# Optimization experiments

Hardware: AMD Instinct MI355X
Metric: run time of the kernel (lower is better)

The kernel has to match this reference:

```python
import jax, jax.numpy as jnp
import numpy as np

DIM = 192
HID = 128
EPS = 1e-8
ITERS = 3
LN_EPS = 1e-5
SCALE = DIM ** (-0.5)


def layer_norm(x, w, b):
    mu = x.mean(axis=-1, keepdims=True)
    var = ((x - mu) ** 2).mean(axis=-1, keepdims=True)
    return (x - mu) * jax.lax.rsqrt(var + LN_EPS) * w + b


def gru_cell(x, h, Wih, Whh, bih, bhh):
    # PyTorch GRUCell: gates ordered (r, z, n)
    gx = x @ Wih.T + bih          # [M, 3*DIM]
    gh = h @ Whh.T + bhh          # [M, 3*DIM]
    xr, xz, xn = jnp.split(gx, 3, axis=-1)
    hr, hz, hn = jnp.split(gh, 3, axis=-1)
    r = jax.nn.sigmoid(xr + hr)
    z = jax.nn.sigmoid(xz + hz)
    n = jnp.tanh(xn + r * hn)
    return (1.0 - z) * n + z * h


def setup_inputs() -> dict:
    key = jax.random.key(0)
    ks = jax.random.split(key, 12)
    B, N, K = 64, 4096, 11
    s = 0.02
    return {
        "inputs": jax.random.normal(ks[0], (B, N, DIM), jnp.float32),
        "noise": jax.random.normal(ks[1], (B, K, DIM), jnp.float32),
        "slots_mu": jax.random.normal(ks[2], (1, 1, DIM), jnp.float32),
        "slots_sigma": jax.random.uniform(ks[3], (1, 1, DIM), jnp.float32),
        "ln_in_w": jnp.ones((DIM,), jnp.float32),
        "ln_in_b": jnp.zeros((DIM,), jnp.float32),
        "ln_slots_w": jnp.ones((DIM,), jnp.float32),
        "ln_slots_b": jnp.zeros((DIM,), jnp.float32),
        "ln_mlp_w": jnp.ones((DIM,), jnp.float32),
        "ln_mlp_b": jnp.zeros((DIM,), jnp.float32),
        "Wq": jax.random.normal(ks[4], (DIM, DIM), jnp.float32) * s,
        "bq": jnp.zeros((DIM,), jnp.float32),
        "Wk": jax.random.normal(ks[5], (DIM, DIM), jnp.float32) * s,
        "bk": jnp.zeros((DIM,), jnp.float32),
        "Wv": jax.random.normal(ks[6], (DIM, DIM), jnp.float32) * s,
        "bv": jnp.zeros((DIM,), jnp.float32),
        "gru_Wih": jax.random.normal(ks[7], (3 * DIM, DIM), jnp.float32) * s,
        "gru_Whh": jax.random.normal(ks[8], (3 * DIM, DIM), jnp.float32) * s,
        "gru_bih": jnp.zeros((3 * DIM,), jnp.float32),
        "gru_bhh": jnp.zeros((3 * DIM,), jnp.float32),
        "mlp_W1": jax.random.normal(ks[9], (DIM, HID), jnp.float32) * s,
        "mlp_b1": jnp.zeros((HID,), jnp.float32),
        "mlp_W2": jax.random.normal(ks[10], (HID, DIM), jnp.float32) * s,
        "mlp_b2": jnp.zeros((DIM,), jnp.float32),
        "n_slots": 11,
    }


def reference(inputs, noise, slots_mu, slots_sigma,
              ln_in_w, ln_in_b, ln_slots_w, ln_slots_b, ln_mlp_w, ln_mlp_b,
              Wq, bq, Wk, bk, Wv, bv,
              gru_Wih, gru_Whh, gru_bih, gru_bhh,
              mlp_W1, mlp_b1, mlp_W2, mlp_b2, n_slots):
    B, N, _ = inputs.shape
    # slots ~ Normal(mu, sigma), reparameterized with fixed noise
    slots = slots_mu + slots_sigma * noise            # [B, K, D]
    x = layer_norm(inputs, ln_in_w, ln_in_b)
    key_vec = x @ Wk + bk                             # [B, N, D]
    val_vec = x @ Wv + bv                             # [B, N, D]
    attn_output = None
    for _ in range(ITERS):
        slots_prev = slots
        s_n = layer_norm(slots, ln_slots_w, ln_slots_b)
        q = s_n @ Wq + bq                             # [B, K, D]
        dots = jnp.einsum('bkd,bnd->bkn', q, key_vec) * SCALE
        attn = jax.nn.softmax(dots, axis=1) + EPS     # softmax over slots axis
        attn_output = attn
        attn = attn / attn.sum(axis=-1, keepdims=True)
        updates = jnp.einsum('bnd,bkn->bkd', val_vec, attn)
        h = gru_cell(updates.reshape(-1, DIM), slots_prev.reshape(-1, DIM),
                     gru_Wih, gru_Whh, gru_bih, gru_bhh)
        slots = h.reshape(B, -1, DIM)
        m = layer_norm(slots, ln_mlp_w, ln_mlp_b)
        m = jax.nn.relu(m @ mlp_W1 + mlp_b1) @ mlp_W2 + mlp_b2
        slots = slots + m
    return (slots, attn_output)
```

## Files before the change

kernel.cpp:

```cpp
#include <hip/hip_runtime.h>
#include <hip/hip_bf16.h>
#include <cstdint>
#include <cstddef>

#define DIM 192
#define NSL 11
#define NB 64
#define NN 4096
#define HIDN 128
#define NCHP 16
#define TROWS 32
#define NT 8
#define LN_EPS 1e-5f
#define EPS_A 1e-8f
#define SCALE_Q 0.07216878364870323f

__device__ __forceinline__ float wred(float v) {
#pragma unroll
  for (int m = 32; m; m >>= 1) v += __shfl_xor(v, m, 64);
  return v;
}

typedef const __attribute__((address_space(1))) void gas_void;
typedef __attribute__((address_space(3))) void las_void;
__device__ __forceinline__ void gload_lds16(const void* g, void* l) {
  __builtin_amdgcn_global_load_lds((gas_void*)g, (las_void*)l, 16, 0, 0);
}

__global__ __launch_bounds__(256) void k_tr(
    const float* __restrict__ Wih, const float* __restrict__ Whh, const float* __restrict__ Wk,
    float* __restrict__ WihT, float* __restrict__ WhhT, float* __restrict__ WkT) {
  __shared__ float t[64][65];
  int tile = blockIdx.x;
  const float* src; float* dst; int R, C;
  if (tile < 27)      { src = Wih; dst = WihT; R = 576; C = 192; }
  else if (tile < 54) { src = Whh; dst = WhhT; R = 576; C = 192; tile -= 27; }
  else                { src = Wk;  dst = WkT;  R = 192; C = 192; tile -= 54; }
  const int ntc = C >> 6;
  const int tr = tile / ntc, tc = tile % ntc;
  const int lane = threadIdx.x & 63, w = threadIdx.x >> 6;
#pragma unroll
  for (int i = 0; i < 16; ++i) {
    int row = w * 16 + i;
    t[row][lane] = src[(size_t)(tr * 64 + row) * C + tc * 64 + lane];
  }
  __syncthreads();
#pragma unroll
  for (int i = 0; i < 16; ++i) {
    int row = w * 16 + i;
    dst[(size_t)(tc * 64 + row) * R + tr * 64 + lane] = t[lane][row];
  }
}

__global__ __launch_bounds__(192) void k_prep(
    const float* __restrict__ lnw, const float* __restrict__ lnb,
    const float* __restrict__ Wq, const float* __restrict__ bq,
    const float* __restrict__ WkT, const float* __restrict__ bk,
    const float* __restrict__ xw, const float* __restrict__ xb,
    const float* __restrict__ noise, const float* __restrict__ mu0, const float* __restrict__ sig,
    float* __restrict__ slots_ws,
    float* __restrict__ qt, float* __restrict__ t0g, float* __restrict__ cpg) {
  const int b = blockIdx.x, kg = blockIdx.y, tid = threadIdx.x;
  const int k0 = kg * 3, kcnt = (kg == 3) ? 2 : 3;
  const int wave = tid >> 6, lane = tid & 63;
  const int j = tid;
  __shared__ __align__(16) float sn[3][DIM];
  __shared__ __align__(16) float qb[3][DIM];
  __shared__ float red[3][3][2];

#pragma unroll
  for (int kk = 0; kk < 3; ++kk) {
    if (kk < kcnt) {
      float v = mu0[j] + sig[j] * noise[(size_t)(b * NSL + k0 + kk) * DIM + j];
      sn[kk][j] = v;
      slots_ws[(size_t)(b * NSL + k0 + kk) * DIM + j] = v;
    } else sn[kk][j] = 0.f;
  }
  __syncthreads();

  for (int kk = wave; kk < 3; kk += 3) {
    float a = sn[kk][lane], c = sn[kk][lane + 64], e = sn[kk][lane + 128];
    float s = wred(a + c + e), ss = wred(a * a + c * c + e * e);
    float mu = s * (1.0f / DIM), var = ss * (1.0f / DIM) - mu * mu;
    float rstd = rsqrtf(var + LN_EPS);
    sn[kk][lane]       = (a - mu) * rstd * lnw[lane]       + lnb[lane];
    sn[kk][lane + 64]  = (c - mu) * rstd * lnw[lane + 64]  + lnb[lane + 64];
    sn[kk][lane + 128] = (e - mu) * rstd * lnw[lane + 128] + lnb[lane + 128];
  }
  __syncthreads();

  float acc[3];
  const float bj = bq[j];
#pragma unroll
  for (int kk = 0; kk < 3; ++kk) acc[kk] = bj;
  for (int d = 0; d < DIM; d += 4) {
    float w0 = Wq[(d + 0) * DIM + j], w1 = Wq[(d + 1) * DIM + j];
    float w2 = Wq[(d + 2) * DIM + j], w3 = Wq[(d + 3) * DIM + j];
#pragma unroll
    for (int kk = 0; kk < 3; ++kk) {
      float4 s4 = *(const float4*)&sn[kk][d];
      acc[kk] = fmaf(s4.w, w3, fmaf(s4.z, w2, fmaf(s4.y, w1, fmaf(s4.x, w0, acc[kk]))));
    }
  }
#pragma unroll
  for (int kk = 0; kk < 3; ++kk) qb[kk][j] = acc[kk];
  __syncthreads();

  float qk[3];
#pragma unroll
  for (int kk = 0; kk < 3; ++kk) qk[kk] = 0.f;
  for (int d = 0; d < DIM; d += 4) {
    float w0 = WkT[(d + 0) * DIM + j], w1 = WkT[(d + 1) * DIM + j];
    float w2 = WkT[(d + 2) * DIM + j], w3 = WkT[(d + 3) * DIM + j];
#pragma unroll
    for (int kk = 0; kk < 3; ++kk) {
      float4 q4 = *(const float4*)&qb[kk][d];
      qk[kk] = fmaf(q4.w, w3, fmaf(q4.z, w2, fmaf(q4.y, w1, fmaf(q4.x, w0, qk[kk]))));
    }
  }
  const float wj = xw[j], bxj = xb[j], bkj = bk[j];
#pragma unroll
  for (int kk = 0; kk < 3; ++kk) {
    float qtv = SCALE_Q * wj * qk[kk];
    if (kk < kcnt) qt[(size_t)(b * NSL + k0 + kk) * DIM + j] = qtv;
    float r1 = wred(qtv);
    float r2 = wred(SCALE_Q * (bxj * qk[kk] + qb[kk][j] * bkj));
    if (lane == 0) { red[wave][kk][0] = r1; red[wave][kk][1] = r2; }
  }
  __syncthreads();
  if (tid < kcnt) {
    t0g[b * NSL + k0 + tid] = red[0][tid][0] + red[1][tid][0] + red[2][tid][0];
    cpg[b * NSL + k0 + tid] = red[0][tid][1] + red[1][tid][1] + red[2][tid][1];
  }
}

__global__ __launch_bounds__(256) __attribute__((amdgpu_waves_per_eu(4, 4))) void k_iter(
    const float* __restrict__ x, const float* __restrict__ qt,
    const float* __restrict__ t0g, const float* __restrict__ cpg,
    float* __restrict__ attn_out, float* __restrict__ P1p,
    float* __restrict__ S_p, float* __restrict__ m1_p) {
  __shared__ __align__(16) float xs[TROWS * DIM];
  __shared__ __align__(16) float qs[NSL * DIM];
  __shared__ __align__(16) float a_lds[TROWS][12];
  __shared__ float rs_lds[TROWS];
  __shared__ float t0s[NSL], cps[NSL];
  __shared__ float redS[4][NSL], redM[4][NSL];

  const int b = blockIdx.x, ch = blockIdx.y, tid = threadIdx.x;
  const int lane = tid & 63, wv = tid >> 6;
  const int widx = tid & 15, g = tid >> 4;

  const float* xbase = x + ((size_t)b * NN + ch * 256) * DIM;

#pragma unroll
  for (int i = 0; i < 6; ++i) {
    int c = i * 4 + wv;
    gload_lds16(xbase + c * 256 + lane * 4, &xs[c * 256]);
  }
  {
    const float4* src = (const float4*)(qt + (size_t)b * NSL * DIM);
    float4* dst = (float4*)qs;
    dst[tid] = src[tid];
    dst[256 + tid] = src[256 + tid];
    if (tid < 16) dst[512 + tid] = src[512 + tid];
  }
  if (tid < NSL) { t0s[tid] = t0g[b * NSL + tid]; cps[tid] = cpg[b * NSL + tid]; }

  float acc[3][NSL], sS[NSL], sM[NSL];
#pragma unroll
  for (int k = 0; k < NSL; ++k) {
    acc[0][k] = 0.f; acc[1][k] = 0.f; acc[2][k] = 0.f;
    sS[k] = 0.f; sM[k] = 0.f;
  }

#pragma unroll 1
  for (int T = 0; T < NT; ++T) {
    if (T == 0) {
      __syncthreads();
    } else {
      __syncthreads();
      const float* src = xbase + (size_t)T * TROWS * DIM;
#pragma unroll
      for (int i = 0; i < 6; ++i) {
        int c = i * 4 + wv;
        gload_lds16(src + c * 256 + lane * 4, &xs[c * 256]);
      }
      asm volatile("s_waitcnt vmcnt(0)" ::: "memory");
      __builtin_amdgcn_s_barrier();
    }

    float dot[2][NSL], st_s[2], st_ss[2];
#pragma unroll
    for (int rr = 0; rr < 2; ++rr) {
      st_s[rr] = 0.f; st_ss[rr] = 0.f;
#pragma unroll
      for (int k = 0; k < NSL; ++k) dot[rr][k] = 0.f;
    }
#pragma unroll
    for (int w = 0; w < 3; ++w) {
      const int c4 = widx + 16 * w;
      float4 xr[2];
#pragma unroll
      for (int rr = 0; rr < 2; ++rr) {
        xr[rr] = ((const float4*)xs)[(2 * g + rr) * 48 + c4];
        st_s[rr] += (xr[rr].x + xr[rr].y) + (xr[rr].z + xr[rr].w);
        st_ss[rr] = fmaf(xr[rr].x, xr[rr].x, fmaf(xr[rr].y, xr[rr].y,
                    fmaf(xr[rr].z, xr[rr].z, fmaf(xr[rr].w, xr[rr].w, st_ss[rr]))));
      }
#pragma unroll
      for (int k = 0; k < NSL; ++k) {
        float4 qv = *(const float4*)&qs[k * DIM + 4 * c4];
#pragma unroll
        for (int rr = 0; rr < 2; ++rr)
          dot[rr][k] = fmaf(xr[rr].w, qv.w, fmaf(xr[rr].z, qv.z,
                       fmaf(xr[rr].y, qv.y, fmaf(xr[rr].x, qv.x, dot[rr][k]))));
      }
    }
#pragma unroll
    for (int m = 1; m <= 8; m <<= 1) {
#pragma unroll
      for (int rr = 0; rr < 2; ++rr) {
        st_s[rr] += __shfl_xor(st_s[rr], m, 64);
        st_ss[rr] += __shfl_xor(st_ss[rr], m, 64);
#pragma unroll
        for (int k = 0; k < NSL; ++k) dot[rr][k] += __shfl_xor(dot[rr][k], m, 64);
      }
    }
    if ((widx & 7) == 0) {
      const int hi = widx >> 3;
      const int r = 2 * g + hi;
      float dsel[NSL];
#pragma unroll
      for (int k = 0; k < NSL; ++k) dsel[k] = (widx == 0) ? dot[0][k] : dot[1][k];
      float sts  = (widx == 0) ? st_s[0]  : st_s[1];
      float stss = (widx == 0) ? st_ss[0] : st_ss[1];
      float mu = sts * (1.0f / DIM);
      float var = stss * (1.0f / DIM) - mu * mu;
      float rstd = rsqrtf(var + LN_EPS);
      float murstd = mu * rstd;
      float dv[NSL];
#pragma unroll
      for (int k = 0; k < NSL; ++k) dv[k] = fmaf(rstd, dsel[k], fmaf(-murstd, t0s[k], cps[k]));
      float mx = dv[0];
#pragma unroll
      for (int k = 1; k < NSL; ++k) mx = fmaxf(mx, dv[k]);
      float es[NSL], sum = 0.f;
#pragma unroll
      for (int k = 0; k < NSL; ++k) { es[k] = __expf(dv[k] - mx); sum += es[k]; }
      float inv = 1.0f / sum;
#pragma unroll
      for (int k = 0; k < NSL; ++k) {
        float a = fmaf(es[k], inv, EPS_A);
        a_lds[r][k] = a;
        sS[k] += a;
        sM[k] = fmaf(a, murstd, sM[k]);
      }
      rs_lds[r] = rstd;
    }
    asm volatile("s_waitcnt lgkmcnt(0)" ::: "memory");
    __builtin_amdgcn_s_barrier();

    {
      int idx = tid;
      attn_out[((size_t)(b * NSL + (idx >> 5))) * NN + ch * 256 + T * TROWS + (idx & 31)]
          = a_lds[idx & 31][idx >> 5];
      idx = tid + 256;
      if (idx < NSL * TROWS)
        attn_out[((size_t)(b * NSL + (idx >> 5))) * NN + ch * 256 + T * TROWS + (idx & 31)]
            = a_lds[idx & 31][idx >> 5];
    }
#pragma unroll 4
    for (int i = 0; i < 8; ++i) {
      const int r = 4 * i + wv;
      float rst = rs_lds[r];
      float4 a0 = *(const float4*)&a_lds[r][0];
      float4 a1 = *(const float4*)&a_lds[r][4];
      float4 a2 = *(const float4*)&a_lds[r][8];
#pragma unroll
      for (int j = 0; j < 3; ++j) {
        const int col = lane + 64 * j;
        float t1 = rst * xs[r * DIM + col];
        acc[j][0]  = fmaf(a0.x, t1, acc[j][0]);
        acc[j][1]  = fmaf(a0.y, t1, acc[j][1]);
        acc[j][2]  = fmaf(a0.z, t1, acc[j][2]);
        acc[j][3]  = fmaf(a0.w, t1, acc[j][3]);
        acc[j][4]  = fmaf(a1.x, t1, acc[j][4]);
        acc[j][5]  = fmaf(a1.y, t1, acc[j][5]);
        acc[j][6]  = fmaf(a1.z, t1, acc[j][6]);
        acc[j][7]  = fmaf(a1.w, t1, acc[j][7]);
        acc[j][8]  = fmaf(a2.x, t1, acc[j][8]);
        acc[j][9]  = fmaf(a2.y, t1, acc[j][9]);
        acc[j][10] = fmaf(a2.z, t1, acc[j][10]);
      }
    }
  }

  __syncthreads();
  float* accbuf = &xs[0];
  const int slot = tid & 127;
  if (wv < 2) {
#pragma unroll
    for (int j = 0; j < 3; ++j)
#pragma unroll
      for (int k = 0; k < NSL; ++k)
        accbuf[slot * 33 + j * 11 + k] = acc[j][k];
  }
  __syncthreads();
  if (wv >= 2) {
#pragma unroll
    for (int j = 0; j < 3; ++j)
#pragma unroll
      for (int k = 0; k < NSL; ++k)
        accbuf[slot * 33 + j * 11 + k] += acc[j][k];
  }
  __syncthreads();
  if (tid < DIM) {
    const int l = tid & 63, j = tid >> 6;
#pragma unroll
    for (int k = 0; k < NSL; ++k) {
      float v = accbuf[l * 33 + j * 11 + k] + accbuf[(64 + l) * 33 + j * 11 + k];
      P1p[(((size_t)b * NCHP + ch) * NSL + k) * DIM + tid] = v;
    }
  }
#pragma unroll
  for (int k = 0; k < NSL; ++k) { sS[k] = wred(sS[k]); sM[k] = wred(sM[k]); }
  if (lane == 0) {
#pragma unroll
    for (int k = 0; k < NSL; ++k) { redS[wv][k] = sS[k]; redM[wv][k] = sM[k]; }
  }
  __syncthreads();
  if (tid < NSL) {
    S_p[((size_t)b * NCHP + ch) * NSL + tid]  = redS[0][tid] + redS[1][tid] + redS[2][tid] + redS[3][tid];
    m1_p[((size_t)b * NCHP + ch) * NSL + tid] = redM[0][tid] + redM[1][tid] + redM[2][tid] + redM[3][tid];
  }
}

#define TPBS 768
__global__ __launch_bounds__(TPBS) void k_step(
    const float* __restrict__ P1p, const float* __restrict__ m1_p, const float* __restrict__ S_p,
    const float* __restrict__ xw, const float* __restrict__ xb,
    const float* __restrict__ Wv, const float* __restrict__ bv,
    const float* __restrict__ slots_in,
    const float* __restrict__ WihT, const float* __restrict__ WhhT,
    const float* __restrict__ bih, const float* __restrict__ bhh,
    const float* __restrict__ mw, const float* __restrict__ mb,
    const float* __restrict__ W1, const float* __restrict__ b1,
    const float* __restrict__ W2, const float* __restrict__ b2,
    const float* __restrict__ sw, const float* __restrict__ sb,
    const float* __restrict__ Wq, const float* __restrict__ bq,
    const float* __restrict__ WkT, const float* __restrict__ bk,
    float* __restrict__ slots_ws, float* __restrict__ slots_out,
    float* __restrict__ qt, float* __restrict__ t0g, float* __restrict__ cpg) {
  const int b = blockIdx.x, kg = blockIdx.y, tid = threadIdx.x;
  const int k0 = kg * 3, kcnt = (kg == 3) ? 2 : 3;
  const int q = tid / 192;
  const int j = tid - q * 192;
  const int lane = tid & 63;

  __shared__ __align__(16) float red[4 * 18 * 192];
  __shared__ __align__(16) float u[3][DIM];
  __shared__ __align__(16) float hp[3][DIM];
  __shared__ __align__(16) float h[3][DIM];
  __shared__ __align__(16) float hid[3][HIDN];
  __shared__ float sSp[3][16], sMp[3][16];
  __shared__ float redw[3][3][2];

#define RED(qq, gg, jj) red[(((qq) * 18 + (gg)) * 192) + (jj)]

  int kidx[3];
#pragma unroll
  for (int kk = 0; kk < 3; ++kk) { int t = k0 + kk; kidx[kk] = t > NSL - 1 ? NSL - 1 : t; }

#pragma unroll
  for (int kk = 0; kk < 3; ++kk) {
    float p = 0.f;
#pragma unroll
    for (int c = 0; c < 4; ++c) {
      int ch = q * 4 + c;
      p += P1p[(((size_t)b * NCHP + ch) * NSL + kidx[kk]) * DIM + j];
    }
    RED(q, kk, j) = p;
  }
  if (tid < 48) {
    int kk = tid >> 4, ch = tid & 15;
    sSp[kk][ch] = S_p[((size_t)b * NCHP + ch) * NSL + kidx[kk]];
    sMp[kk][ch] = m1_p[((size_t)b * NCHP + ch) * NSL + kidx[kk]];
  }
  if (q == 0) {
#pragma unroll
    for (int kk = 0; kk < 3; ++kk)
      hp[kk][j] = slots_in[(size_t)(b * NSL + kidx[kk]) * DIM + j];
  }
  __syncthreads();
  if (tid < 576) {
    const int kk = q;
    float p = RED(0, kk, j) + RED(1, kk, j) + RED(2, kk, j) + RED(3, kk, j);
    float S = 0.f, M = 0.f;
#pragma unroll
    for (int ch = 0; ch < 16; ++ch) { S += sSp[kk][ch]; M += sMp[kk][ch]; }
    u[kk][j] = xw[j] * (p - M) / S + xb[j];
  }
  __syncthreads();

  {
    float p0 = 0.f, p1 = 0.f, p2 = 0.f;
    const int d0 = q * 48;
#pragma unroll 4
    for (int d = d0; d < d0 + 48; ++d) {
      float w = Wv[d * DIM + j];
      p0 = fmaf(u[0][d], w, p0);
      p1 = fmaf(u[1][d], w, p1);
      p2 = fmaf(u[2][d], w, p2);
    }
    RED(q, 0, j) = p0; RED(q, 1, j) = p1; RED(q, 2, j) = p2;
  }
  __syncthreads();
  if (tid < 576) {
    const int kk = q;
    u[kk][j] = bv[j] + RED(0, kk, j) + RED(1, kk, j) + RED(2, kk, j) + RED(3, kk, j);
  }
  __syncthreads();

  {
    float pxr[3] = {0,0,0}, pxz[3] = {0,0,0}, pxn[3] = {0,0,0};
    float phr[3] = {0,0,0}, phz[3] = {0,0,0}, phn[3] = {0,0,0};
    const int d0 = q * 48;
#pragma unroll 2
    for (int d = d0; d < d0 + 48; ++d) {
      const float* ihrow = WihT + (size_t)d * 576;
      const float* hhrow = WhhT + (size_t)d * 576;
      float ar = ihrow[j], az = ihrow[192 + j], an = ihrow[384 + j];
      float br = hhrow[j], bz = hhrow[192 + j], bn = hhrow[384 + j];
#pragma unroll
      for (int kk = 0; kk < 3; ++kk) {
        float uv = u[kk][d], pv = hp[kk][d];
        pxr[kk] = fmaf(uv, ar, pxr[kk]);
        pxz[kk] = fmaf(uv, az, pxz[kk]);
        pxn[kk] = fmaf(uv, an, pxn[kk]);
        phr[kk] = fmaf(pv, br, phr[kk]);
        phz[kk] = fmaf(pv, bz, phz[kk]);
        phn[kk] = fmaf(pv, bn, phn[kk]);
      }
    }
#pragma unroll
    for (int kk = 0; kk < 3; ++kk) {
      RED(q, 0 + kk, j)  = pxr[kk];  RED(q, 3 + kk, j)  = pxz[kk];
      RED(q, 6 + kk, j)  = pxn[kk];  RED(q, 9 + kk, j)  = phr[kk];
      RED(q, 12 + kk, j) = phz[kk];  RED(q, 15 + kk, j) = phn[kk];
    }
  }
  __syncthreads();
  if (tid < 576) {
    const int kk = q;
    float xr = bih[j]       + RED(0,0+kk,j)  + RED(1,0+kk,j)  + RED(2,0+kk,j)  + RED(3,0+kk,j);
    float xz = bih[192 + j] + RED(0,3+kk,j)  + RED(1,3+kk,j)  + RED(2,3+kk,j)  + RED(3,3+kk,j);
    float xn = bih[384 + j] + RED(0,6+kk,j)  + RED(1,6+kk,j)  + RED(2,6+kk,j)  + RED(3,6+kk,j);
    float hr = bhh[j]       + RED(0,9+kk,j)  + RED(1,9+kk,j)  + RED(2,9+kk,j)  + RED(3,9+kk,j);
    float hz = bhh[192 + j] + RED(0,12+kk,j) + RED(1,12+kk,j) + RED(2,12+kk,j) + RED(3,12+kk,j);
    float hn = bhh[384 + j] + RED(0,15+kk,j) + RED(1,15+kk,j) + RED(2,15+kk,j) + RED(3,15+kk,j);
    float r = 1.f / (1.f + __expf(-(xr + hr)));
    float z = 1.f / (1.f + __expf(-(xz + hz)));
    float n = tanhf(xn + r * hn);
    h[kk][j] = (1.f - z) * n + z * hp[kk][j];
  }
  __syncthreads();

  {
    const int wv = tid >> 6;
    if (wv < 3) {
      const int kk = wv;
      float a = h[kk][lane], c = h[kk][lane + 64], e = h[kk][lane + 128];
      float s = wred(a + c + e), ss = wred(a * a + c * c + e * e);
      float mu = s * (1.0f / DIM), var = ss * (1.0f / DIM) - mu * mu;
      float rstd = rsqrtf(var + LN_EPS);
      u[kk][lane]       = (a - mu) * rstd * mw[lane]       + mb[lane];
      u[kk][lane + 64]  = (c - mu) * rstd * mw[lane + 64]  + mb[lane + 64];
      u[kk][lane + 128] = (e - mu) * rstd * mw[lane + 128] + mb[lane + 128];
    }
  }
  __syncthreads();

  if (j < HIDN) {
    float p0 = 0.f, p1 = 0.f, p2 = 0.f;
    const int d0 = q * 48;
#pragma unroll 4
    for (int d = d0; d < d0 + 48; ++d) {
      float w = W1[d * HIDN + j];
      p0 = fmaf(u[0][d], w, p0);
      p1 = fmaf(u[1][d], w, p1);
      p2 = fmaf(u[2][d], w, p2);
    }
    RED(q, 0, j) = p0; RED(q, 1, j) = p1; RED(q, 2, j) = p2;
  }
  __syncthreads();
  if (tid < 576 && j < HIDN) {
    const int kk = q;
    float v = b1[j] + RED(0, kk, j) + RED(1, kk, j) + RED(2, kk, j) + RED(3, kk, j);
    hid[kk][j] = fmaxf(v, 0.f);
  }
  __syncthreads();

  {
    float p0 = 0.f, p1 = 0.f, p2 = 0.f;
    const int c0 = q * 32;
#pragma unroll 4
    for (int c = c0; c < c0 + 32; ++c) {
      float w = W2[c * DIM + j];
      p0 = fmaf(hid[0][c], w, p0);
      p1 = fmaf(hid[1][c], w, p1);
      p2 = fmaf(hid[2][c], w, p2);
    }
    RED(q, 0, j) = p0; RED(q, 1, j) = p1; RED(q, 2, j) = p2;
  }
  __syncthreads();
  if (tid < 576) {
    const int kk = q;
    float outv = h[kk][j] + b2[j] + RED(0, kk, j) + RED(1, kk, j) + RED(2, kk, j) + RED(3, kk, j);
    if (kk < kcnt) {
      size_t gi = (size_t)(b * NSL + k0 + kk) * DIM + j;
      slots_ws[gi] = outv;
      slots_out[gi] = outv;
    }
    hp[kk][j] = outv;
  }
  __syncthreads();

  {
    const int wv = tid >> 6;
    if (wv < 3) {
      const int kk = wv;
      float a = hp[kk][lane], c = hp[kk][lane + 64], e = hp[kk][lane + 128];
      float s = wred(a + c + e), ss = wred(a * a + c * c + e * e);
      float mu = s * (1.0f / DIM), var = ss * (1.0f / DIM) - mu * mu;
      float rstd = rsqrtf(var + LN_EPS);
      u[kk][lane]       = (a - mu) * rstd * sw[lane]       + sb[lane];
      u[kk][lane + 64]  = (c - mu) * rstd * sw[lane + 64]  + sb[lane + 64];
      u[kk][lane + 128] = (e - mu) * rstd * sw[lane + 128] + sb[lane + 128];
    }
  }
  __syncthreads();

  {
    float p0 = 0.f, p1 = 0.f, p2 = 0.f;
    const int d0 = q * 48;
#pragma unroll 4
    for (int d = d0; d < d0 + 48; ++d) {
      float w = Wq[d * DIM + j];
      p0 = fmaf(u[0][d], w, p0);
      p1 = fmaf(u[1][d], w, p1);
      p2 = fmaf(u[2][d], w, p2);
    }
    RED(q, 0, j) = p0; RED(q, 1, j) = p1; RED(q, 2, j) = p2;
  }
  __syncthreads();
  if (tid < 576) {
    const int kk = q;
    h[kk][j] = bq[j] + RED(0, kk, j) + RED(1, kk, j) + RED(2, kk, j) + RED(3, kk, j);
  }
  __syncthreads();

  {
    float p0 = 0.f, p1 = 0.f, p2 = 0.f;
    const int d0 = q * 48;
#pragma unroll 4
    for (int d = d0; d < d0 + 48; ++d) {
      float w = WkT[d * DIM + j];
      p0 = fmaf(h[0][d], w, p0);
      p1 = fmaf(h[1][d], w, p1);
      p2 = fmaf(h[2][d], w, p2);
    }
    RED(q, 0, j) = p0; RED(q, 1, j) = p1; RED(q, 2, j) = p2;
  }
  __syncthreads();
  if (tid < 576) {
    const int kk = q;
    u[kk][j] = RED(0, kk, j) + RED(1, kk, j) + RED(2, kk, j) + RED(3, kk, j);
  }
  __syncthreads();
  if (tid < 192) {
    const int wv = tid >> 6;
    const float wxj = xw[j], bxj = xb[j], bkj = bk[j];
#pragma unroll
    for (int kk = 0; kk < 3; ++kk) {
      float qk = u[kk][j];
      float qv = h[kk][j];
      float qtv = SCALE_Q * wxj * qk;
      if (kk < kcnt) qt[(size_t)(b * NSL + k0 + kk) * DIM + j] = qtv;
      float r1 = wred(qtv);
      float r2 = wred(SCALE_Q * (bxj * qk + qv * bkj));
      if (lane == 0) { redw[wv][kk][0] = r1; redw[wv][kk][1] = r2; }
    }
  }
  __syncthreads();
  if (tid < kcnt) {
    t0g[b * NSL + k0 + tid] = redw[0][tid][0] + redw[1][tid][0] + redw[2][tid][0];
    cpg[b * NSL + k0 + tid] = redw[0][tid][1] + redw[1][tid][1] + redw[2][tid][1];
  }
#undef RED
}

extern "C" void kernel_launch(void* const* d_in, const int* in_sizes, int n_in,
                              void* d_out, int out_size, void* d_ws, size_t ws_size,
                              hipStream_t stream) {
  const float* inputs      = (const float*)d_in[0];
  const float* noise       = (const float*)d_in[1];
  const float* slots_mu    = (const float*)d_in[2];
  const float* slots_sigma = (const float*)d_in[3];
  const float* ln_in_w     = (const float*)d_in[4];
  const float* ln_in_b     = (const float*)d_in[5];
  const float* ln_slots_w  = (const float*)d_in[6];
  const float* ln_slots_b  = (const float*)d_in[7];
  const float* ln_mlp_w    = (const float*)d_in[8];
  const float* ln_mlp_b    = (const float*)d_in[9];
  const float* Wq  = (const float*)d_in[10];
  const float* bq  = (const float*)d_in[11];
  const float* Wk  = (const float*)d_in[12];
  const float* bk  = (const float*)d_in[13];
  const float* Wv  = (const float*)d_in[14];
  const float* bv  = (const float*)d_in[15];
  const float* Wih = (const float*)d_in[16];
  const float* Whh = (const float*)d_in[17];
  const float* bih = (const float*)d_in[18];
  const float* bhh = (const float*)d_in[19];
  const float* W1  = (const float*)d_in[20];
  const float* b1  = (const float*)d_in[21];
  const float* W2  = (const float*)d_in[22];
  const float* b2  = (const float*)d_in[23];

  float* out = (float*)d_out;
  float* slots_out = out;
  float* attn_out  = out + NB * NSL * DIM;

  char* w = (char*)d_ws;
  float* slots = (float*)w;
  float* qt    = (float*)(w + 540672);
  float* t0g   = (float*)(w + 1081344);
  float* cpg   = (float*)(w + 1084160);
  float* P1p   = (float*)(w + 1086976);
  float* S_p   = (float*)(w + 9737728);
  float* m1_p  = (float*)(w + 9782784);
  float* WihT  = (float*)(w + 9827840);
  float* WhhT  = (float*)(w + 10270208);
  float* WkT   = (float*)(w + 10712576);

  k_tr<<<63, 256, 0, stream>>>(Wih, Whh, Wk, WihT, WhhT, WkT);
  k_prep<<<dim3(NB, 4), 192, 0, stream>>>(ln_slots_w, ln_slots_b, Wq, bq, WkT, bk,
                                          ln_in_w, ln_in_b, noise, slots_mu, slots_sigma,
                                          slots, qt, t0g, cpg);
  for (int it = 0; it < 3; ++it) {
    k_iter<<<dim3(NB, NCHP), 256, 0, stream>>>(inputs, qt, t0g, cpg, attn_out, P1p, S_p, m1_p);
    k_step<<<dim3(NB, 4), TPBS, 0, stream>>>(P1p, m1_p, S_p, ln_in_w, ln_in_b, Wv, bv, slots,
                                             WihT, WhhT, bih, bhh, ln_mlp_w, ln_mlp_b,
                                             W1, b1, W2, b2, ln_slots_w, ln_slots_b,
                                             Wq, bq, WkT, bk, slots, slots_out, qt, t0g, cpg);
  }
}
```

Measured before the change: 695.0 us.

## Specialize waves: three accumulate attn-weighted x, one writes attn and slot sums

Restructures the k_iter accumulation phase. Three waves (192 threads) each own one feature column and accumulate over all 32 rows, so per-thread accumulator state drops from 33 to 11 values. The fourth wave writes attn_out and computes the per-slot sums from LDS, which removes the cross-wave LDS reduction, the extra barriers and the shuffle reductions at the end. The waves_per_eu constraint is also removed, since register pressure is lower. The risk is imbalance: the fourth wave does little FMA work while the other three each do more rows.

```diff
diff --git a/kernel.cpp b/kernel.cpp
--- a/kernel.cpp
+++ b/kernel.cpp
@@ -134,7 +134,7 @@
   }
 }
 
-__global__ __launch_bounds__(256) __attribute__((amdgpu_waves_per_eu(4, 4))) void k_iter(
+__global__ __launch_bounds__(256) void k_iter(
     const float* __restrict__ x, const float* __restrict__ qt,
     const float* __restrict__ t0g, const float* __restrict__ cpg,
     float* __restrict__ attn_out, float* __restrict__ P1p,
@@ -143,11 +143,11 @@
   __shared__ __align__(16) float qs[NSL * DIM];
   __shared__ __align__(16) float a_lds[TROWS][12];
   __shared__ float rs_lds[TROWS];
+  __shared__ float mr_lds[TROWS];
   __shared__ float t0s[NSL], cps[NSL];
-  __shared__ float redS[4][NSL], redM[4][NSL];
 
   const int b = blockIdx.x, ch = blockIdx.y, tid = threadIdx.x;
-  const int lane = tid & 63, wv = tid >> 6;
+  const int wv = tid >> 6;
   const int widx = tid & 15, g = tid >> 4;
 
   const float* xbase = x + ((size_t)b * NN + ch * 256) * DIM;
@@ -155,7 +155,7 @@
 #pragma unroll
   for (int i = 0; i < 6; ++i) {
     int c = i * 4 + wv;
-    gload_lds16(xbase + c * 256 + lane * 4, &xs[c * 256]);
+    gload_lds16(xbase + c * 256 + (tid & 63) * 4, &xs[c * 256]);
   }
   {
     const float4* src = (const float4*)(qt + (size_t)b * NSL * DIM);
@@ -166,12 +166,10 @@
   }
   if (tid < NSL) { t0s[tid] = t0g[b * NSL + tid]; cps[tid] = cpg[b * NSL + tid]; }
 
-  float acc[3][NSL], sS[NSL], sM[NSL];
-#pragma unroll
-  for (int k = 0; k < NSL; ++k) {
-    acc[0][k] = 0.f; acc[1][k] = 0.f; acc[2][k] = 0.f;
-    sS[k] = 0.f; sM[k] = 0.f;
-  }
+  float acc[NSL];
+  float sSa = 0.f, sMa = 0.f;
+#pragma unroll
+  for (int k = 0; k < NSL; ++k) acc[k] = 0.f;
 
 #pragma unroll 1
   for (int T = 0; T < NT; ++T) {
@@ -183,7 +181,7 @@
 #pragma unroll
       for (int i = 0; i < 6; ++i) {
         int c = i * 4 + wv;
-        gload_lds16(src + c * 256 + lane * 4, &xs[c * 256]);
+        gload_lds16(src + c * 256 + (tid & 63) * 4, &xs[c * 256]);
       }
       asm volatile("s_waitcnt vmcnt(0)" ::: "memory");
       __builtin_amdgcn_s_barrier();
@@ -249,89 +247,60 @@
       for (int k = 0; k < NSL; ++k) { es[k] = __expf(dv[k] - mx); sum += es[k]; }
       float inv = 1.0f / sum;
 #pragma unroll
-      for (int k = 0; k < NSL; ++k) {
-        float a = fmaf(es[k], inv, EPS_A);
-        a_lds[r][k] = a;
-        sS[k] += a;
-        sM[k] = fmaf(a, murstd, sM[k]);
-      }
+      for (int k = 0; k < NSL; ++k) a_lds[r][k] = fmaf(es[k], inv, EPS_A);
       rs_lds[r] = rstd;
+      mr_lds[r] = murstd;
     }
     asm volatile("s_waitcnt lgkmcnt(0)" ::: "memory");
     __builtin_amdgcn_s_barrier();
 
-    {
-      int idx = tid;
-      attn_out[((size_t)(b * NSL + (idx >> 5))) * NN + ch * 256 + T * TROWS + (idx & 31)]
-          = a_lds[idx & 31][idx >> 5];
-      idx = tid + 256;
-      if (idx < NSL * TROWS)
-        attn_out[((size_t)(b * NSL + (idx >> 5))) * NN + ch * 256 + T * TROWS + (idx & 31)]
-            = a_lds[idx & 31][idx >> 5];
-    }
+    if (tid < 192) {
 #pragma unroll 4
-    for (int i = 0; i < 8; ++i) {
-      const int r = 4 * i + wv;
-      float rst = rs_lds[r];
-      float4 a0 = *(const float4*)&a_lds[r][0];
-      float4 a1 = *(const float4*)&a_lds[r][4];
-      float4 a2 = *(const float4*)&a_lds[r][8];
-#pragma unroll
-      for (int j = 0; j < 3; ++j) {
-        const int col = lane + 64 * j;
-        float t1 = rst * xs[r * DIM + col];
-        acc[j][0]  = fmaf(a0.x, t1, acc[j][0]);
-        acc[j][1]  = fmaf(a0.y, t1, acc[j][1]);
-        acc[j][2]  = fmaf(a0.z, t1, acc[j][2]);
-        acc[j][3]  = fmaf(a0.w, t1, acc[j][3]);
-        acc[j][4]  = fmaf(a1.x, t1, acc[j][4]);
-        acc[j][5]  = fmaf(a1.y, t1, acc[j][5]);
-        acc[j][6]  = fmaf(a1.z, t1, acc[j][6]);
-        acc[j][7]  = fmaf(a1.w, t1, acc[j][7]);
-        acc[j][8]  = fmaf(a2.x, t1, acc[j][8]);
-        acc[j][9]  = fmaf(a2.y, t1, acc[j][9]);
-        acc[j][10] = fmaf(a2.z, t1, acc[j][10]);
-      }
-    }
-  }
-
-  __syncthreads();
-  float* accbuf = &xs[0];
-  const int slot = tid & 127;
-  if (wv < 2) {
-#pragma unroll
-    for (int j = 0; j < 3; ++j)
-#pragma unroll
-      for (int k = 0; k < NSL; ++k)
-        accbuf[slot * 33 + j * 11 + k] = acc[j][k];
-  }
-  __syncthreads();
-  if (wv >= 2) {
-#pragma unroll
-    for (int j = 0; j < 3; ++j)
-#pragma unroll
-      for (int k = 0; k < NSL; ++k)
-        accbuf[slot * 33 + j * 11 + k] += acc[j][k];
-  }
-  __syncthreads();
-  if (tid < DIM) {
-    const int l = tid & 63, j = tid >> 6;
-#pragma unroll
-    for (int k = 0; k < NSL; ++k) {
-      float v = accbuf[l * 33 + j * 11 + k] + accbuf[(64 + l) * 33 + j * 11 + k];
-      P1p[(((size_t)b * NCHP + ch) * NSL + k) * DIM + tid] = v;
-    }
-  }
-#pragma unroll
-  for (int k = 0; k < NSL; ++k) { sS[k] = wred(sS[k]); sM[k] = wred(sM[k]); }
-  if (lane == 0) {
-#pragma unroll
-    for (int k = 0; k < NSL; ++k) { redS[wv][k] = sS[k]; redM[wv][k] = sM[k]; }
-  }
-  __syncthreads();
-  if (tid < NSL) {
-    S_p[((size_t)b * NCHP + ch) * NSL + tid]  = redS[0][tid] + redS[1][tid] + redS[2][tid] + redS[3][tid];
-    m1_p[((size_t)b * NCHP + ch) * NSL + tid] = redM[0][tid] + redM[1][tid] + redM[2][tid] + redM[3][tid];
+      for (int r = 0; r < TROWS; ++r) {
+        float t1 = rs_lds[r] * xs[r * DIM + tid];
+        float4 a0 = *(const float4*)&a_lds[r][0];
+        float4 a1 = *(const float4*)&a_lds[r][4];
+        float4 a2 = *(const float4*)&a_lds[r][8];
+        acc[0]  = fmaf(a0.x, t1, acc[0]);
+        acc[1]  = fmaf(a0.y, t1, acc[1]);
+        acc[2]  = fmaf(a0.z, t1, acc[2]);
+        acc[3]  = fmaf(a0.w, t1, acc[3]);
+        acc[4]  = fmaf(a1.x, t1, acc[4]);
+        acc[5]  = fmaf(a1.y, t1, acc[5]);
+        acc[6]  = fmaf(a1.z, t1, acc[6]);
+        acc[7]  = fmaf(a1.w, t1, acc[7]);
+        acc[8]  = fmaf(a2.x, t1, acc[8]);
+        acc[9]  = fmaf(a2.y, t1, acc[9]);
+        acc[10] = fmaf(a2.z, t1, acc[10]);
+      }
+    } else {
+      const int t = tid - 192;
+#pragma unroll
+      for (int i = 0; i < 6; ++i) {
+        int idx = t + 64 * i;
+        if (idx < NSL * TROWS)
+          attn_out[((size_t)(b * NSL + (idx >> 5))) * NN + ch * 256 + T * TROWS + (idx & 31)]
+              = a_lds[idx & 31][idx >> 5];
+      }
+      if (t < NSL) {
+#pragma unroll 4
+        for (int r = 0; r < TROWS; ++r) {
+          float a = a_lds[r][t];
+          sSa += a;
+          sMa = fmaf(a, mr_lds[r], sMa);
+        }
+      }
+    }
+  }
+
+  if (tid < 192) {
+#pragma unroll
+    for (int k = 0; k < NSL; ++k)
+      P1p[(((size_t)b * NCHP + ch) * NSL + k) * DIM + tid] = acc[k];
+  } else if (tid - 192 < NSL) {
+    const int t = tid - 192;
+    S_p[((size_t)b * NCHP + ch) * NSL + t]  = sSa;
+    m1_p[((size_t)b * NCHP + ch) * NSL + t] = sMa;
   }
 }
 
```

Result: no change. 694.3 us (-0.1%).
